# Performance work log

Measured on AMD Instinct MI355X. Metric: run time of the kernel, lower is better.

Reference implementation:

```python
import jax, jax.numpy as jnp
import numpy as np
import math

NUM_EXPERTS = 8
MIN_EXPERTS_ACTIVE = 2  # max(1, 8 // 4) per __init__ formula


def setup_inputs() -> dict:
    key = jax.random.key(0)
    ks = jax.random.split(key, 6)
    N, Cin, H, W = 16384, 68, 8, 8
    Cproj = 128
    patch = jax.random.normal(ks[0], (N, Cin, H, W), dtype=jnp.float32)
    conv_w = jax.random.normal(ks[1], (Cproj, Cin, 3, 3), dtype=jnp.float32) * (1.0 / np.sqrt(Cin * 9))
    conv_b = jnp.zeros((Cproj,), dtype=jnp.float32)
    fc_w = jax.random.normal(ks[2], (Cproj, NUM_EXPERTS), dtype=jnp.float32) * (1.0 / np.sqrt(Cproj))
    fc_b = jnp.zeros((NUM_EXPERTS,), dtype=jnp.float32)
    wth_max_c = jnp.float32(0.4)
    wth_entropy_c = jnp.float32(0.3)
    wth_gap_c = jnp.float32(0.3)
    threshold = jnp.float32(0.2)
    return {
        'patch': patch, 'conv_w': conv_w, 'conv_b': conv_b,
        'fc_w': fc_w, 'fc_b': fc_b,
        'wth_max_c': wth_max_c, 'wth_entropy_c': wth_entropy_c, 'wth_gap_c': wth_gap_c,
        'threshold': threshold, 'layer_idx': 0, 'current_epoch': 30,
    }


def _gate(patch, conv_w, conv_b, fc_w, fc_b):
    # 3x3 SAME conv (NCHW) -> ReLU -> global avg pool -> linear
    y = jax.lax.conv_general_dilated(
        patch, conv_w, window_strides=(1, 1), padding='SAME',
        dimension_numbers=('NCHW', 'OIHW', 'NCHW'))
    y = jax.nn.relu(y + conv_b[None, :, None, None])
    pooled = y.mean(axis=(2, 3))  # [N, Cproj]
    return pooled @ fc_w + fc_b   # [N, E]


def _compute_gap(sw):
    # sw: [N, E] sorted descending
    k = min(4, NUM_EXPERTS - 1)
    mean_rest = sw[:, 1:k + 1].mean(axis=-1, keepdims=True)
    gap = (sw[:, 0:1] - mean_rest) / (sw[:, 0:1] + 1e-8)
    return jnp.clip(gap, 0.0, 1.0)


def _adaptive_threshold(w, base_threshold, wth_max_c, wth_entropy_c, wth_gap_c):
    sw = -jnp.sort(-w, axis=-1)  # descending
    max_component = 1.0 - sw[:, 0:1]
    mean_w = w.mean(axis=-1, keepdims=True)
    std_w = w.std(axis=-1, keepdims=True, ddof=1)  # torch default unbiased
    entropy = -(w * jnp.log(w + 1e-18)).sum(axis=-1, keepdims=True)
    entropy_component = 1.0 - entropy / math.log(NUM_EXPERTS)
    gap_component = _compute_gap(sw)
    adaptive_factor = (wth_max_c * max_component + wth_entropy_c * entropy_component
                       + wth_gap_c * gap_component)
    th = base_threshold * (0.5 + adaptive_factor)
    min_th = jnp.maximum(jnp.float32(0.05), mean_w - 0.5 * std_w)
    max_th = jnp.minimum(jnp.float32(0.7), sw[:, 0:1] - 0.1 * std_w)
    th = jnp.clip(th, min_th, max_th)
    kth = sw[:, MIN_EXPERTS_ACTIVE - 1:MIN_EXPERTS_ACTIVE]
    return jnp.minimum(th, kth * 0.9)


def reference(patch, conv_w, conv_b, fc_w, fc_b,
              wth_max_c, wth_entropy_c, wth_gap_c,
              threshold, layer_idx, current_epoch):
    logits = _gate(patch, conv_w, conv_b, fc_w, fc_b)
    weights = jax.nn.softmax(logits, axis=-1)
    th = _adaptive_threshold(weights, threshold, wth_max_c, wth_entropy_c, wth_gap_c)
    if current_epoch is not None and current_epoch < 20:
        weights_norm = jnp.ones_like(weights) / NUM_EXPERTS
    elif current_epoch is not None and 20 <= current_epoch <= 25:
        tau = max(0.1, 1.0 - (current_epoch - 20) * 0.18)
        s = jax.nn.sigmoid((weights - th) / tau)
        weights_norm = s / jnp.clip(s.sum(axis=-1, keepdims=True), 1e-8)
    else:  # current_epoch > 25 or eval: straight-through hard/soft masking
        tau = 0.1
        hard = (weights > th).astype(weights.dtype)
        soft = jax.nn.sigmoid((weights - th) / tau)
        filtered = hard + jax.lax.stop_gradient(soft - hard)
        weights_norm = filtered / jnp.clip(filtered.sum(axis=-1, keepdims=True), 1e-8)
    return weights_norm
```

## Files before the change

### kernel.cpp

```cpp
#include <hip/hip_runtime.h>


typedef _Float16 half8 __attribute__((ext_vector_type(8)));
typedef float    floatx4 __attribute__((ext_vector_type(4)));

#define A_SAMPLE  14400
#define LDS_P_OFF 28800
#define LDS_TOTAL 29824

__global__ void prep_weights(const float* __restrict__ cw, _Float16* __restrict__ Bw) {
  int i  = blockIdx.x * 256 + threadIdx.x;
  int h  = (i >= 43008) ? 1 : 0;
  int r1 = i - h * 43008;
  int c  = r1 >> 11;
  int r2 = r1 & 2047;
  int l  = r2 >> 5;
  int r3 = r2 & 31;
  int n  = r3 >> 3;
  int j  = r3 & 7;
  int quad = l >> 4, lane15 = l & 15;
  int col  = h * 64 + n * 16 + lane15;
  int kdim = (c * 4 + quad) * 8 + j;
  int kb   = kdim >> 3;
  int s    = (kb * 57) >> 9;
  int ci   = kdim - s * 72;
  float v = 0.f;
  if (s < 9 && ci < 68) {
    int ky = s / 3, kx = s - 3 * ky;
    v = cw[((col * 68 + ci) * 3 + ky) * 3 + kx];
  }
  Bw[i] = (_Float16)v;
}

__global__ __launch_bounds__(256, 4) void router_main(
    const float* __restrict__ patch,
    const float* __restrict__ conv_b,
    const _Float16* __restrict__ Bw,
    const float* __restrict__ fc_w,
    const float* __restrict__ fc_b,
    const float* __restrict__ p_wmax,
    const float* __restrict__ p_went,
    const float* __restrict__ p_wgap,
    const float* __restrict__ p_thr,
    const int* __restrict__ p_epoch,
    float* __restrict__ out)
{
  __shared__ __align__(16) unsigned char lds[LDS_TOTAL];
  const int tid    = threadIdx.x;
  const int l      = tid & 63;
  const int w      = tid >> 6;
  const int lane15 = l & 15;
  const int quad   = l >> 4;
  const int sm     = w >> 1;
  const int h      = w & 1;
  const int n0     = h * 64;
  const int n_s    = blockIdx.x * 2;

  {
    unsigned char* abase = lds + sm * A_SAMPLE;
    float4 z4 = make_float4(0.f, 0.f, 0.f, 0.f);
    #pragma unroll
    for (int j0 = 0; j0 < 3; ++j0) {
      int jj = j0 * 64 + l;
      if (jj < 162) {
        int j   = h * 162 + jj;
        int ri  = j / 9;
        int col = j - ri * 9;
        int row = (ri < 10) ? ri
                : (ri < 26) ? ((((ri - 10) >> 1) + 1) * 10 + ((ri - 10) & 1) * 9)
                            : (ri + 64);
        *(float4*)(abase + row * 144 + col * 16) = z4;
      }
    }
  }
  {
    const float* psrc = patch + (size_t)(n_s + sm) * 4352 + l;
    int y = l >> 3, x = l & 7;
    unsigned char* arow = lds + sm * A_SAMPLE + ((y + 1) * 10 + (x + 1)) * 144;
    #pragma unroll
    for (int bb = 0; bb < 5; ++bb) {
      int b = bb * 2 + h;
      if (b < 9) {
        half8 hh;
        #pragma unroll
        for (int j = 0; j < 8; ++j) {
          int ci = b * 8 + j;
          float v = (ci < 68) ? psrc[ci * 64] : 0.f;
          hh[j] = (_Float16)v;
        }
        *(half8*)(arow + b * 16) = hh;
      }
    }
  }
  __syncthreads();

  int apos[4];
  #pragma unroll
  for (int t = 0; t < 4; ++t) {
    int p  = t * 16 + lane15;
    int pp = ((p >> 3) + 1) * 10 + (p & 7) + 1;
    apos[t] = sm * A_SAMPLE + pp * 144;
  }

  const _Float16* bb = Bw + h * 43008 + l * 32;

  floatx4 acc[4][4];
  floatx4 zacc = {0.f, 0.f, 0.f, 0.f};
  #pragma unroll
  for (int t = 0; t < 4; ++t)
    #pragma unroll
    for (int n = 0; n < 4; ++n) acc[t][n] = zacc;

  half8 bcur[4];
  #pragma unroll
  for (int n = 0; n < 4; ++n) bcur[n] = *(const half8*)(bb + n * 8);

  #pragma unroll 1
  for (int c = 0; c < 20; ++c) {
    half8 bnext[4];
    #pragma unroll
    for (int n = 0; n < 4; ++n)
      bnext[n] = *(const half8*)(bb + (c + 1) * 2048 + n * 8);

    int kb  = c * 4 + quad;
    int s   = (kb * 57) >> 9;
    int rem = kb - s * 9;
    int dy  = (s * 11) >> 5;
    int dx  = s - 3 * dy;
    int roff = (dy * 10 + dx - 11) * 144 + rem * 16;

    half8 afr[4];
    #pragma unroll
    for (int t = 0; t < 4; ++t)
      afr[t] = *(const half8*)(lds + apos[t] + roff);

    #pragma unroll
    for (int t = 0; t < 4; ++t)
      #pragma unroll
      for (int n = 0; n < 4; ++n)
        acc[t][n] = __builtin_amdgcn_mfma_f32_16x16x32_f16(afr[t], bcur[n], acc[t][n], 0, 0, 0);

    #pragma unroll
    for (int n = 0; n < 4; ++n) bcur[n] = bnext[n];
  }

  {
    int roff = (quad == 0) ? 1712 : 0;
    half8 afr[4];
    #pragma unroll
    for (int t = 0; t < 4; ++t)
      afr[t] = *(const half8*)(lds + apos[t] + roff);
    #pragma unroll
    for (int t = 0; t < 4; ++t)
      #pragma unroll
      for (int n = 0; n < 4; ++n)
        acc[t][n] = __builtin_amdgcn_mfma_f32_16x16x32_f16(afr[t], bcur[n], acc[t][n], 0, 0, 0);
  }

  float bcoef[4];
  #pragma unroll
  for (int n = 0; n < 4; ++n) bcoef[n] = conv_b[n0 + n * 16 + lane15];

  float* pl = (float*)(lds + LDS_P_OFF);
  #pragma unroll
  for (int n = 0; n < 4; ++n) {
    float ssum = 0.f;
    #pragma unroll
    for (int t = 0; t < 4; ++t)
      #pragma unroll
      for (int r = 0; r < 4; ++r)
        ssum += fmaxf(acc[t][n][r] + bcoef[n], 0.f);
    ssum += __shfl_xor(ssum, 16);
    ssum += __shfl_xor(ssum, 32);
    if (l < 16)
      pl[sm * 128 + n0 + n * 16 + lane15] = ssum * (1.f / 64.f);
  }
  __syncthreads();

  if (w < 2) {
    const float* plw = pl + w * 128;
    int e  = l >> 3;
    int c8 = l & 7;
    float part = 0.f;
    #pragma unroll
    for (int m = 0; m < 16; ++m) {
      int co = c8 + 8 * m;
      part += plw[co] * fc_w[co * 8 + e];
    }
    part += __shfl_xor(part, 1);
    part += __shfl_xor(part, 2);
    part += __shfl_xor(part, 4);

    float lg[8];
    #pragma unroll
    for (int j = 0; j < 8; ++j) lg[j] = __shfl(part, j * 8) + fc_b[j];

    float mx = lg[0];
    #pragma unroll
    for (int j = 1; j < 8; ++j) mx = fmaxf(mx, lg[j]);
    float wgt[8]; float sum = 0.f;
    #pragma unroll
    for (int j = 0; j < 8; ++j) { wgt[j] = expf(lg[j] - mx); sum += wgt[j]; }
    float inv = 1.f / sum;
    #pragma unroll
    for (int j = 0; j < 8; ++j) wgt[j] *= inv;

    float sw[8];
    #pragma unroll
    for (int j = 0; j < 8; ++j) sw[j] = wgt[j];
    #define CSD(i, j) { float hi_ = fmaxf(sw[i], sw[j]); float lo_ = fminf(sw[i], sw[j]); sw[i] = hi_; sw[j] = lo_; }
    CSD(0,1) CSD(2,3) CSD(4,5) CSD(6,7)
    CSD(0,2) CSD(1,3) CSD(4,6) CSD(5,7)
    CSD(1,2) CSD(5,6)
    CSD(0,4) CSD(1,5) CSD(2,6) CSD(3,7)
    CSD(2,4) CSD(3,5)
    CSD(1,2) CSD(3,4) CSD(5,6)
    #undef CSD

    float s1 = 0.f;
    #pragma unroll
    for (int j = 0; j < 8; ++j) s1 += wgt[j];
    float mean = s1 * 0.125f;
    float var = 0.f;
    #pragma unroll
    for (int j = 0; j < 8; ++j) { float d = wgt[j] - mean; var += d * d; }
    float stdv = sqrtf(var * (1.f / 7.f));
    float ent = 0.f;
    #pragma unroll
    for (int j = 0; j < 8; ++j) ent -= wgt[j] * logf(wgt[j] + 1e-18f);

    float maxc  = 1.f - sw[0];
    float entc  = 1.f - ent * 0.48089834696298783f;
    float mrest = (sw[1] + sw[2] + sw[3] + sw[4]) * 0.25f;
    float gap   = (sw[0] - mrest) / (sw[0] + 1e-8f);
    gap = fminf(fmaxf(gap, 0.f), 1.f);
    float af = p_wmax[0] * maxc + p_went[0] * entc + p_wgap[0] * gap;
    float th = p_thr[0] * (0.5f + af);
    float mn  = fmaxf(0.05f, mean - 0.5f * stdv);
    float mxt = fminf(0.7f, sw[0] - 0.1f * stdv);
    th = fminf(fmaxf(th, mn), mxt);
    th = fminf(th, sw[1] * 0.9f);

    int epoch = p_epoch[0];
    float outv[8];
    if (epoch < 20) {
      #pragma unroll
      for (int j = 0; j < 8; ++j) outv[j] = 0.125f;
    } else {
      float tau = (epoch <= 25) ? fmaxf(0.1f, 1.0f - (float)(epoch - 20) * 0.18f) : 0.1f;
      float ssum = 0.f;
      #pragma unroll
      for (int j = 0; j < 8; ++j) {
        float sj = 1.f / (1.f + expf(-(wgt[j] - th) / tau));
        outv[j] = sj; ssum += sj;
      }
      float invs = 1.f / fmaxf(ssum, 1e-8f);
      #pragma unroll
      for (int j = 0; j < 8; ++j) outv[j] *= invs;
    }

    if (l < 8) {
      float mv = outv[0];
      #pragma unroll
      for (int j = 1; j < 8; ++j) mv = (l == j) ? outv[j] : mv;
      out[(n_s + w) * 8 + l] = mv;
    }
  }
}

extern "C" void kernel_launch(void* const* d_in, const int* in_sizes, int n_in,
                              void* d_out, int out_size, void* d_ws, size_t ws_size,
                              hipStream_t stream) {
  const float* patch  = (const float*)d_in[0];
  const float* conv_w = (const float*)d_in[1];
  const float* conv_b = (const float*)d_in[2];
  const float* fc_w   = (const float*)d_in[3];
  const float* fc_b   = (const float*)d_in[4];
  const float* wmax   = (const float*)d_in[5];
  const float* went   = (const float*)d_in[6];
  const float* wgap   = (const float*)d_in[7];
  const float* thr    = (const float*)d_in[8];
  const int*   epoch  = (const int*)d_in[10];
  float* outp = (float*)d_out;
  _Float16* Bw = (_Float16*)d_ws;

  int N = in_sizes[0] / 4352;
  prep_weights<<<336, 256, 0, stream>>>(conv_w, Bw);
  router_main<<<N / 2, 256, 0, stream>>>(patch, conv_b, Bw, fc_w, fc_b,
                                         wmax, went, wgap, thr, epoch, outp);
}
```

Before: 536.9 us.

## Double-buffer A/B MFMA fragments and prefetch first weight chunk before barrier

Unrolls the K loop by two and ping-pongs two register sets of A (LDS) and B (global) fragments, so loads for the next chunk are issued before the current chunk's MFMAs. The first B chunk is now fetched before the LDS barrier to hide global latency behind patch staging. The tail chunk is folded in through a clamped offset helper. Launch bounds drop from 4 to 3 waves per SIMD so the extra fragment registers fit, which trades occupancy for more in-flight loads per wave.

```diff
diff --git a/kernel.cpp b/kernel.cpp
--- a/kernel.cpp
+++ b/kernel.cpp
@@ -32,7 +32,17 @@
   Bw[i] = (_Float16)v;
 }
 
-__global__ __launch_bounds__(256, 4) void router_main(
+__device__ __forceinline__ int roff_of(int cc, int quad) {
+  int kb = cc * 4 + quad;
+  kb = (kb > 80) ? 80 : kb;
+  int s   = (kb * 57) >> 9;
+  int rem = kb - s * 9;
+  int dy  = (s * 11) >> 5;
+  int dx  = s - 3 * dy;
+  return (dy * 10 + dx - 11) * 144 + rem * 16;
+}
+
+__global__ __launch_bounds__(256, 3) void router_main(
     const float* __restrict__ patch,
     const float* __restrict__ conv_b,
     const _Float16* __restrict__ Bw,
@@ -92,6 +102,12 @@
       }
     }
   }
+
+  const _Float16* bb = Bw + h * 43008 + l * 32;
+  half8 b0[4], b1[4];
+  #pragma unroll
+  for (int n = 0; n < 4; ++n) b0[n] = *(const half8*)(bb + n * 8);
+
   __syncthreads();
 
   int apos[4];
@@ -102,8 +118,6 @@
     apos[t] = sm * A_SAMPLE + pp * 144;
   }
 
-  const _Float16* bb = Bw + h * 43008 + l * 32;
-
   floatx4 acc[4][4];
   floatx4 zacc = {0.f, 0.f, 0.f, 0.f};
   #pragma unroll
@@ -111,51 +125,52 @@
     #pragma unroll
     for (int n = 0; n < 4; ++n) acc[t][n] = zacc;
 
-  half8 bcur[4];
-  #pragma unroll
-  for (int n = 0; n < 4; ++n) bcur[n] = *(const half8*)(bb + n * 8);
+  half8 a0[4], a1[4];
+  {
+    int ro = roff_of(0, quad);
+    #pragma unroll
+    for (int t = 0; t < 4; ++t)
+      a0[t] = *(const half8*)(lds + apos[t] + ro);
+  }
 
   #pragma unroll 1
-  for (int c = 0; c < 20; ++c) {
-    half8 bnext[4];
+  for (int c = 0; c < 20; c += 2) {
+    {
+      #pragma unroll
+      for (int n = 0; n < 4; ++n)
+        b1[n] = *(const half8*)(bb + (c + 1) * 2048 + n * 8);
+      int ro = roff_of(c + 1, quad);
+      #pragma unroll
+      for (int t = 0; t < 4; ++t)
+        a1[t] = *(const half8*)(lds + apos[t] + ro);
+    }
+    #pragma unroll
+    for (int t = 0; t < 4; ++t)
+      #pragma unroll
+      for (int n = 0; n < 4; ++n)
+        acc[t][n] = __builtin_amdgcn_mfma_f32_16x16x32_f16(a0[t], b0[n], acc[t][n], 0, 0, 0);
+
+    {
+      #pragma unroll
+      for (int n = 0; n < 4; ++n)
+        b0[n] = *(const half8*)(bb + (c + 2) * 2048 + n * 8);
+      int ro = roff_of(c + 2, quad);
+      #pragma unroll
+      for (int t = 0; t < 4; ++t)
+        a0[t] = *(const half8*)(lds + apos[t] + ro);
+    }
+    #pragma unroll
+    for (int t = 0; t < 4; ++t)
+      #pragma unroll
+      for (int n = 0; n < 4; ++n)
+        acc[t][n] = __builtin_amdgcn_mfma_f32_16x16x32_f16(a1[t], b1[n], acc[t][n], 0, 0, 0);
+  }
+
+  #pragma unroll
+  for (int t = 0; t < 4; ++t)
     #pragma unroll
     for (int n = 0; n < 4; ++n)
-      bnext[n] = *(const half8*)(bb + (c + 1) * 2048 + n * 8);
-
-    int kb  = c * 4 + quad;
-    int s   = (kb * 57) >> 9;
-    int rem = kb - s * 9;
-    int dy  = (s * 11) >> 5;
-    int dx  = s - 3 * dy;
-    int roff = (dy * 10 + dx - 11) * 144 + rem * 16;
-
-    half8 afr[4];
-    #pragma unroll
-    for (int t = 0; t < 4; ++t)
-      afr[t] = *(const half8*)(lds + apos[t] + roff);
-
-    #pragma unroll
-    for (int t = 0; t < 4; ++t)
-      #pragma unroll
-      for (int n = 0; n < 4; ++n)
-        acc[t][n] = __builtin_amdgcn_mfma_f32_16x16x32_f16(afr[t], bcur[n], acc[t][n], 0, 0, 0);
-
-    #pragma unroll
-    for (int n = 0; n < 4; ++n) bcur[n] = bnext[n];
-  }
-
-  {
-    int roff = (quad == 0) ? 1712 : 0;
-    half8 afr[4];
-    #pragma unroll
-    for (int t = 0; t < 4; ++t)
-      afr[t] = *(const half8*)(lds + apos[t] + roff);
-    #pragma unroll
-    for (int t = 0; t < 4; ++t)
-      #pragma unroll
-      for (int n = 0; n < 4; ++n)
-        acc[t][n] = __builtin_amdgcn_mfma_f32_16x16x32_f16(afr[t], bcur[n], acc[t][n], 0, 0, 0);
-  }
+      acc[t][n] = __builtin_amdgcn_mfma_f32_16x16x32_f16(a0[t], b0[n], acc[t][n], 0, 0, 0);
 
   float bcoef[4];
   #pragma unroll
```

New measurement: 544.3 us. Within noise of the previous version (+1.4%).
